# Kernel optimization log

Hardware: AMD Instinct MI355X
Metric: run time of the kernel (lower is better)

The kernel has to match this reference:

```python
import jax, jax.numpy as jnp
import numpy as np
from jax import lax

B, L, STEPS = 64, 512, 20


def setup_inputs() -> dict:
    key = jax.random.key(0)
    k1, k2, k3, k4 = jax.random.split(key, 4)
    scores = jax.random.uniform(k1, (B, L, L), dtype=jnp.float32)
    # M is a hard 0/1 constraint mask in the original pipeline; make it binary + symmetric
    m_raw = jax.random.uniform(k2, (B, L, L), dtype=jnp.float32)
    M = (m_raw > 0.5).astype(jnp.float32)
    M = jnp.maximum(M, jnp.swapaxes(M, 1, 2))
    return {
        "scores": scores,
        "M": M,
        "s": jnp.float32(0.5),
        "w": jax.random.uniform(k3, (1,), dtype=jnp.float32),
        "rho_p": jax.random.uniform(k4, (L, L), dtype=jnp.float32),
        "alpha": jnp.float32(0.005),
        "belt": jnp.float32(0.05),
        "lr_alpha": jnp.float32(0.99),
        "lr_belt": jnp.float32(0.99),
    }


def reference(scores, M, s, w, rho_p, alpha, belt, lr_alpha, lr_belt):
    relu = jax.nn.relu

    def sym(x):  # (x + x^T)/2 * M, transpose over the two seq dims
        return (x + jnp.swapaxes(x, 1, 2)) * 0.5 * M

    U = scores - s                      # [B,L,L]
    A_hat = scores
    A = sym(A_hat)
    Lm = w * relu(jnp.sum(A, axis=-1) - 1.0)  # [B,L]

    def step(carry, t):
        Lm, A, A_hat = carry
        row_dev = jnp.sum(A, axis=-1) - 1.0                      # [B,L]
        G = U * 0.5 - (Lm * jnp.sign(row_dev))[:, :, None]       # broadcast replaces repeat
        a_t = alpha * jnp.power(lr_alpha, t)
        A_hat2 = A_hat + a_t * A_hat * M * (G + jnp.swapaxes(G, 1, 2))
        A_hat2 = relu(jnp.abs(A_hat2) - rho_p * a_t)
        A_hat2 = 1.0 - relu(1.0 - A_hat2)                        # clip above at 1
        A2 = sym(A_hat2)
        Lm2 = Lm + belt * jnp.power(lr_belt, t) * relu(jnp.sum(A2, axis=-1) - 1.0)
        return (Lm2, A2, A_hat2), None

    ts = jnp.arange(STEPS, dtype=scores.dtype)
    (Lm, A, A_hat), _ = lax.scan(step, (Lm, A, A_hat), ts)
    return A
```

## Files before the change

kernel.cpp:

```cpp
#include <hip/hip_runtime.h>
#include <cstdint>
#include <cstddef>

#define LDIM 512
#define BATCH 64
#define NSTEPS 20
#define NTHREADS 256
#define PTHREADS 512
#define SLABS 8
#define BPB 8
#define CNT_STRIDE 16

using f4 = __attribute__((ext_vector_type(4))) float;
using h4 = __attribute__((ext_vector_type(4))) _Float16;

#define MU_MASKED (-1024.0f)
#define MU_THRESH (-512.0f)

__device__ __forceinline__ float relu_f(float x) { return fmaxf(x, 0.0f); }
__device__ __forceinline__ float sign_f(float x) {
  return (x > 0.0f) ? 1.0f : ((x < 0.0f) ? -1.0f : 0.0f);
}
__device__ __forceinline__ float wave_reduce_sum(float v) {
  v += __shfl_xor(v, 32);
  v += __shfl_xor(v, 16);
  v += __shfl_xor(v, 8);
  v += __shfl_xor(v, 4);
  v += __shfl_xor(v, 2);
  v += __shfl_xor(v, 1);
  return v;
}
__device__ __forceinline__ void st_agent(float* p, float v) {
  __hip_atomic_store(p, v, __ATOMIC_RELAXED, __HIP_MEMORY_SCOPE_AGENT);
}
__device__ __forceinline__ float ld_agent(const float* p) {
  return __hip_atomic_load(p, __ATOMIC_RELAXED, __HIP_MEMORY_SCOPE_AGENT);
}

__global__ __launch_bounds__(NTHREADS) void k_build(
    const float* __restrict__ scores, const float* __restrict__ M,
    const float* __restrict__ s_ptr, _Float16* __restrict__ MU,
    unsigned int* __restrict__ counter) {
  __shared__ float Sa[64][65];
  __shared__ float Sb[64][65];
  if (blockIdx.x < BATCH && threadIdx.x == 0) counter[blockIdx.x * CNT_STRIDE] = 0u;
  const int b = blockIdx.x / 36;
  int rem = blockIdx.x % 36;
  int ti = 0;
  while (rem >= 8 - ti) {
    rem -= 8 - ti;
    ti++;
  }
  const int tj = ti + rem;
  const int tid = threadIdx.x;
  const int c = tid & 63;
  const int r0 = tid >> 6;
  const float sval = s_ptr[0];
  const size_t mb = (size_t)b * LDIM * LDIM;
#pragma unroll
  for (int k = 0; k < 16; k++) {
    const int r = 4 * k + r0;
    Sa[r][c] = scores[mb + (size_t)(ti * 64 + r) * LDIM + tj * 64 + c];
    Sb[r][c] = scores[mb + (size_t)(tj * 64 + r) * LDIM + ti * 64 + c];
  }
  __syncthreads();
#pragma unroll
  for (int k = 0; k < 16; k++) {
    const int r = 4 * k + r0;
    const size_t idx_ij = mb + (size_t)(ti * 64 + r) * LDIM + tj * 64 + c;
    const float mij = M[idx_ij];
    const float us = 0.5f * (Sa[r][c] + Sb[c][r]) - sval;
    MU[idx_ij] = (_Float16)((mij != 0.0f) ? us : MU_MASKED);
    if (ti != tj) {
      const size_t idx_ji = mb + (size_t)(tj * 64 + r) * LDIM + ti * 64 + c;
      const float mji = M[idx_ji];
      const float usj = 0.5f * (Sb[r][c] + Sa[c][r]) - sval;
      MU[idx_ji] = (_Float16)((mji != 0.0f) ? usj : MU_MASKED);
    }
  }
}

__global__ __launch_bounds__(NTHREADS) void k_rho(const float* __restrict__ rho,
                                                  _Float16* __restrict__ rho_h) {
  const int idx = (blockIdx.x * NTHREADS + threadIdx.x) * 4;
  const f4 v = *(const f4*)(rho + idx);
  h4 o;
#pragma unroll
  for (int k = 0; k < 4; k++) o[k] = (_Float16)v[k];
  *(h4*)(rho_h + idx) = o;
}

__global__ __launch_bounds__(PTHREADS, 2) void k_persist(
    const float* __restrict__ scores, const _Float16* __restrict__ MU,
    const _Float16* __restrict__ rho_h, const float* __restrict__ w_ptr,
    const float* __restrict__ alpha_ptr, const float* __restrict__ belt_ptr,
    const float* __restrict__ lra_ptr, const float* __restrict__ lrb_ptr,
    float* __restrict__ rowpart, float* __restrict__ colpart,
    unsigned int* __restrict__ counter, float* __restrict__ Ah) {
  __shared__ _Float16 muL[64][LDIM];
  __shared__ float stage[4][LDIM];
  __shared__ float lmsgS[LDIM];

  const int tid = threadIdx.x;
  const int lane = tid & 63;
  const int w = tid >> 6;
  const int b = blockIdx.x >> 3;
  const int sb = blockIdx.x & 7;
  const int wrow = sb * 64 + w * 8;
  const int j0 = lane << 2;
  const size_t mb = (size_t)b * LDIM * LDIM;

  const float wv = w_ptr[0];
  const float belt = belt_ptr[0];
  const float lra = lra_ptr[0];
  const float lrb = lrb_ptr[0];
  float at = alpha_ptr[0];
  float lrbp = 1.0f;
  float lm_reg = 0.0f;

  const size_t RP = (size_t)BATCH * LDIM;
  const size_t CP = (size_t)BATCH * SLABS * LDIM;
  unsigned int* const cnt = counter + b * CNT_STRIDE;

  f4 ahv[8][2];
  float colacc[8];

#define ARRIVE_WAIT(tgt)                                                       \
  do {                                                                         \
    __syncthreads();                                                           \
    if (tid == 0) {                                                            \
      __hip_atomic_fetch_add(cnt, 1u, __ATOMIC_RELEASE,                        \
                             __HIP_MEMORY_SCOPE_AGENT);                        \
      while (__hip_atomic_load(cnt, __ATOMIC_RELAXED,                          \
                               __HIP_MEMORY_SCOPE_AGENT) < (tgt))              \
        __builtin_amdgcn_s_sleep(8);                                           \
    }                                                                          \
    __syncthreads();                                                           \
  } while (0)

#define COLREDUCE_STORE(dstp)                                                  \
  do {                                                                         \
    if (w < 4) {                                                               \
      f4 sa = {colacc[0], colacc[1], colacc[2], colacc[3]};                    \
      f4 sbv = {colacc[4], colacc[5], colacc[6], colacc[7]};                   \
      *(f4*)&stage[w][j0] = sa;                                                \
      *(f4*)&stage[w][256 + j0] = sbv;                                         \
    }                                                                          \
    __syncthreads();                                                           \
    if (w >= 4) {                                                              \
      f4 sa = *(f4*)&stage[w - 4][j0];                                         \
      f4 sbv = *(f4*)&stage[w - 4][256 + j0];                                  \
      sa[0] += colacc[0]; sa[1] += colacc[1];                                  \
      sa[2] += colacc[2]; sa[3] += colacc[3];                                  \
      sbv[0] += colacc[4]; sbv[1] += colacc[5];                                \
      sbv[2] += colacc[6]; sbv[3] += colacc[7];                                \
      *(f4*)&stage[w - 4][j0] = sa;                                            \
      *(f4*)&stage[w - 4][256 + j0] = sbv;                                     \
    }                                                                          \
    __syncthreads();                                                           \
    {                                                                          \
      float cs = stage[0][tid] + stage[1][tid] + stage[2][tid] +               \
                 stage[3][tid];                                                \
      st_agent((dstp) + tid, cs);                                              \
    }                                                                          \
  } while (0)

#pragma unroll
  for (int k = 0; k < 8; k++) colacc[k] = 0.0f;
#pragma unroll
  for (int r = 0; r < 8; r++) {
    const int i = wrow + r;
    const size_t base = mb + (size_t)i * LDIM;
    const f4 s0 = *(const f4*)(scores + base + j0);
    const f4 s1 = *(const f4*)(scores + base + 256 + j0);
    const h4 m0 = *(const h4*)(MU + base + j0);
    const h4 m1 = *(const h4*)(MU + base + 256 + j0);
    ahv[r][0] = s0;
    ahv[r][1] = s1;
    const int lr = (w << 3) + r;
    *(h4*)&muL[lr][j0] = m0;
    *(h4*)&muL[lr][256 + j0] = m1;
    float rowc = 0.0f;
#pragma unroll
    for (int k = 0; k < 4; k++) {
      const float c0v = ((float)m0[k] > MU_THRESH) ? s0[k] : 0.0f;
      const float c1v = ((float)m1[k] > MU_THRESH) ? s1[k] : 0.0f;
      rowc += c0v + c1v;
      colacc[k] += c0v;
      colacc[4 + k] += c1v;
    }
    const float rsum = wave_reduce_sum(rowc);
    if (lane == 0) st_agent(rowpart + (size_t)b * LDIM + i, rsum);
  }
  COLREDUCE_STORE(colpart + ((size_t)b * SLABS + sb) * LDIM);
  ARRIVE_WAIT((unsigned)BPB);

  for (int sp = 0; sp < NSTEPS; ++sp) {
    const int par = sp & 1;
    {
      const int i = tid;
      const float rsum = ld_agent(rowpart + (size_t)par * RP + (size_t)b * LDIM + i);
      const float* cb = colpart + (size_t)par * CP + (size_t)b * SLABS * LDIM + i;
      float csum = 0.0f;
#pragma unroll
      for (int s2 = 0; s2 < SLABS; s2++) csum += ld_agent(cb + (size_t)s2 * LDIM);
      const float rd = 0.5f * (rsum + csum) - 1.0f;
      float lm;
      if (sp == 0)
        lm = wv * relu_f(rd);
      else
        lm = lm_reg + belt * lrbp * relu_f(rd);
      lm_reg = lm;
      lmsgS[i] = lm * sign_f(rd);
    }
    __syncthreads();

    const f4 lmja = *(const f4*)&lmsgS[j0];
    const f4 lmjb = *(const f4*)&lmsgS[256 + j0];
    const bool last = (sp == NSTEPS - 1);
    const float rat = at;
#pragma unroll
    for (int k = 0; k < 8; k++) colacc[k] = 0.0f;

#pragma unroll
    for (int r = 0; r < 8; r++) {
      const int i = wrow + r;
      const int lr = (w << 3) + r;
      const float lmi = lmsgS[i];
      const h4 mh0 = *(const h4*)&muL[lr][j0];
      const h4 mh1 = *(const h4*)&muL[lr][256 + j0];
      const h4 rh0 = *(const h4*)(rho_h + (size_t)i * LDIM + j0);
      const h4 rh1 = *(const h4*)(rho_h + (size_t)i * LDIM + 256 + j0);
      float rowc = 0.0f;
#pragma unroll
      for (int k = 0; k < 4; k++) {
        const float mva = (float)mh0[k];
        const bool ma = mva > MU_THRESH;
        const float ga = ma ? (mva - lmi - lmja[k]) : 0.0f;
        const float ua = ahv[r][0][k] * fmaf(rat, ga, 1.0f);
        const float va = fminf(relu_f(fabsf(ua) - (float)rh0[k] * rat), 1.0f);
        ahv[r][0][k] = va;
        const float ca = ma ? va : 0.0f;
        rowc += ca;
        colacc[k] += ca;
        const float mvb = (float)mh1[k];
        const bool mbk = mvb > MU_THRESH;
        const float gb = mbk ? (mvb - lmi - lmjb[k]) : 0.0f;
        const float ub = ahv[r][1][k] * fmaf(rat, gb, 1.0f);
        const float vb = fminf(relu_f(fabsf(ub) - (float)rh1[k] * rat), 1.0f);
        ahv[r][1][k] = vb;
        const float cbv = mbk ? vb : 0.0f;
        rowc += cbv;
        colacc[4 + k] += cbv;
      }
      if (!last) {
        const float rsum = wave_reduce_sum(rowc);
        if (lane == 0)
          st_agent(rowpart + (size_t)(par ^ 1) * RP + (size_t)b * LDIM + i, rsum);
      }
    }
    if (!last) {
      COLREDUCE_STORE(colpart + (size_t)(par ^ 1) * CP +
                      ((size_t)b * SLABS + sb) * LDIM);
      ARRIVE_WAIT((unsigned)BPB * (unsigned)(sp + 2));
    }
    at *= lra;
    if (sp > 0) lrbp *= lrb;
  }

#pragma unroll
  for (int r = 0; r < 8; r++) {
    const size_t base = mb + (size_t)(wrow + r) * LDIM;
    *(f4*)(Ah + base + j0) = ahv[r][0];
    *(f4*)(Ah + base + 256 + j0) = ahv[r][1];
  }
#undef ARRIVE_WAIT
#undef COLREDUCE_STORE
}

__global__ __launch_bounds__(NTHREADS) void k_final(float* __restrict__ Ah,
                                                    const float* __restrict__ M) {
  __shared__ float At[64][65];
  __shared__ float Bt[64][65];
  const int b = blockIdx.x / 36;
  int rem = blockIdx.x % 36;
  int ti = 0;
  while (rem >= 8 - ti) {
    rem -= 8 - ti;
    ti++;
  }
  const int tj = ti + rem;
  const int tid = threadIdx.x;
  const int c = tid & 63;
  const int r0 = tid >> 6;
  const size_t mb = (size_t)b * LDIM * LDIM;

#pragma unroll
  for (int k = 0; k < 16; k++) {
    const int r = 4 * k + r0;
    At[r][c] = Ah[mb + (size_t)(ti * 64 + r) * LDIM + tj * 64 + c];
    Bt[r][c] = Ah[mb + (size_t)(tj * 64 + r) * LDIM + ti * 64 + c];
  }
  __syncthreads();
#pragma unroll
  for (int k = 0; k < 16; k++) {
    const int r = 4 * k + r0;
    const size_t idx_ij = mb + (size_t)(ti * 64 + r) * LDIM + tj * 64 + c;
    const float mij = M[idx_ij];
    Ah[idx_ij] = 0.5f * (At[r][c] + Bt[c][r]) * mij;
    if (ti != tj) {
      const size_t idx_ji = mb + (size_t)(tj * 64 + r) * LDIM + ti * 64 + c;
      const float mji = M[idx_ji];
      Ah[idx_ji] = 0.5f * (Bt[r][c] + At[c][r]) * mji;
    }
  }
}

extern "C" void kernel_launch(void* const* d_in, const int* in_sizes, int n_in,
                              void* d_out, int out_size, void* d_ws,
                              size_t ws_size, hipStream_t stream) {
  const float* scores = (const float*)d_in[0];
  const float* M = (const float*)d_in[1];
  const float* s_p = (const float*)d_in[2];
  const float* w_p = (const float*)d_in[3];
  const float* rho = (const float*)d_in[4];
  const float* alpha_p = (const float*)d_in[5];
  const float* belt_p = (const float*)d_in[6];
  const float* lra_p = (const float*)d_in[7];
  const float* lrb_p = (const float*)d_in[8];
  float* Ah = (float*)d_out;

  char* ws = (char*)d_ws;
  size_t off = 0;
  auto walloc = [&](size_t bytes) -> void* {
    void* p = (void*)(ws + off);
    off += (bytes + 255) & ~(size_t)255;
    return p;
  };
  const size_t NEL = (size_t)BATCH * LDIM * LDIM;
  _Float16* MU = (_Float16*)walloc(NEL * 2);
  _Float16* rho_h = (_Float16*)walloc((size_t)LDIM * LDIM * 2);
  float* rowpart = (float*)walloc((size_t)2 * BATCH * LDIM * 4);
  float* colpart = (float*)walloc((size_t)2 * BATCH * SLABS * LDIM * 4);
  unsigned int* cnt = (unsigned int*)walloc(BATCH * CNT_STRIDE * 4);
  (void)in_sizes;
  (void)n_in;
  (void)out_size;
  (void)ws_size;

  k_build<<<dim3(BATCH * 36), dim3(NTHREADS), 0, stream>>>(scores, M, s_p, MU,
                                                           cnt);
  k_rho<<<dim3(LDIM * LDIM / (NTHREADS * 4)), dim3(NTHREADS), 0, stream>>>(
      rho, rho_h);

  k_persist<<<dim3(BATCH * BPB), dim3(PTHREADS), 0, stream>>>(
      scores, MU, rho_h, w_p, alpha_p, belt_p, lra_p, lrb_p, rowpart, colpart,
      cnt, Ah);

  k_final<<<dim3(BATCH * 36), dim3(NTHREADS), 0, stream>>>(Ah, M);
}
```

Measured before the change: 542.3 us.

## Use 1024-thread persistent blocks, fuse rho conversion into build, vectorize build

The persistent kernel now runs 4 blocks of 1024 threads per batch, each holding 128 rows, instead of 8 blocks of 512. This halves the column-partial slabs and the number of blocks taking part in each per-batch barrier, but doubles the shared MU tile to 128 KB per block. The rho fp16 conversion is folded into k_build to drop one launch, and k_build's loads and stores now use 4-wide vectors with padded shared tiles. Sched barriers are added inside the row loops. The larger LDS footprint may cut occupancy, since launch_bounds still requests 2 blocks per CU.

```diff
diff --git a/kernel.cpp b/kernel.cpp
--- a/kernel.cpp
+++ b/kernel.cpp
@@ -6,9 +6,8 @@
 #define BATCH 64
 #define NSTEPS 20
 #define NTHREADS 256
-#define PTHREADS 512
-#define SLABS 8
-#define BPB 8
+#define PTHREADS 1024
+#define BPB 4
 #define CNT_STRIDE 16
 
 using f4 = __attribute__((ext_vector_type(4))) float;
@@ -40,10 +39,20 @@
 __global__ __launch_bounds__(NTHREADS) void k_build(
     const float* __restrict__ scores, const float* __restrict__ M,
     const float* __restrict__ s_ptr, _Float16* __restrict__ MU,
+    const float* __restrict__ rho, _Float16* __restrict__ rho_h,
     unsigned int* __restrict__ counter) {
-  __shared__ float Sa[64][65];
-  __shared__ float Sb[64][65];
-  if (blockIdx.x < BATCH && threadIdx.x == 0) counter[blockIdx.x * CNT_STRIDE] = 0u;
+  __shared__ float Sa[64][68];
+  __shared__ float Sb[64][68];
+  const int tid = threadIdx.x;
+  if (blockIdx.x < BATCH && tid == 0) counter[blockIdx.x * CNT_STRIDE] = 0u;
+  if (blockIdx.x < 256) {
+    const int idx = (blockIdx.x * NTHREADS + tid) * 4;
+    const f4 v = *(const f4*)(rho + idx);
+    h4 o;
+#pragma unroll
+    for (int k = 0; k < 4; k++) o[k] = (_Float16)v[k];
+    *(h4*)(rho_h + idx) = o;
+  }
   const int b = blockIdx.x / 36;
   int rem = blockIdx.x % 36;
   int ti = 0;
@@ -52,42 +61,44 @@
     ti++;
   }
   const int tj = ti + rem;
-  const int tid = threadIdx.x;
-  const int c = tid & 63;
-  const int r0 = tid >> 6;
+  const int cg = tid & 15;
+  const int rr = tid >> 4;
+  const int c4 = cg * 4;
   const float sval = s_ptr[0];
   const size_t mb = (size_t)b * LDIM * LDIM;
 #pragma unroll
-  for (int k = 0; k < 16; k++) {
-    const int r = 4 * k + r0;
-    Sa[r][c] = scores[mb + (size_t)(ti * 64 + r) * LDIM + tj * 64 + c];
-    Sb[r][c] = scores[mb + (size_t)(tj * 64 + r) * LDIM + ti * 64 + c];
+  for (int p = 0; p < 4; p++) {
+    const int r = p * 16 + rr;
+    *(f4*)&Sa[r][c4] =
+        *(const f4*)(scores + mb + (size_t)(ti * 64 + r) * LDIM + tj * 64 + c4);
+    *(f4*)&Sb[r][c4] =
+        *(const f4*)(scores + mb + (size_t)(tj * 64 + r) * LDIM + ti * 64 + c4);
   }
   __syncthreads();
 #pragma unroll
-  for (int k = 0; k < 16; k++) {
-    const int r = 4 * k + r0;
-    const size_t idx_ij = mb + (size_t)(ti * 64 + r) * LDIM + tj * 64 + c;
-    const float mij = M[idx_ij];
-    const float us = 0.5f * (Sa[r][c] + Sb[c][r]) - sval;
-    MU[idx_ij] = (_Float16)((mij != 0.0f) ? us : MU_MASKED);
+  for (int p = 0; p < 4; p++) {
+    const int r = p * 16 + rr;
+    const size_t idx_ij = mb + (size_t)(ti * 64 + r) * LDIM + tj * 64 + c4;
+    const f4 mij = *(const f4*)(M + idx_ij);
+    h4 o;
+#pragma unroll
+    for (int k = 0; k < 4; k++) {
+      const float us = 0.5f * (Sa[r][c4 + k] + Sb[c4 + k][r]) - sval;
+      o[k] = (_Float16)((mij[k] != 0.0f) ? us : MU_MASKED);
+    }
+    *(h4*)(MU + idx_ij) = o;
     if (ti != tj) {
-      const size_t idx_ji = mb + (size_t)(tj * 64 + r) * LDIM + ti * 64 + c;
-      const float mji = M[idx_ji];
-      const float usj = 0.5f * (Sb[r][c] + Sa[c][r]) - sval;
-      MU[idx_ji] = (_Float16)((mji != 0.0f) ? usj : MU_MASKED);
-    }
-  }
-}
-
-__global__ __launch_bounds__(NTHREADS) void k_rho(const float* __restrict__ rho,
-                                                  _Float16* __restrict__ rho_h) {
-  const int idx = (blockIdx.x * NTHREADS + threadIdx.x) * 4;
-  const f4 v = *(const f4*)(rho + idx);
-  h4 o;
-#pragma unroll
-  for (int k = 0; k < 4; k++) o[k] = (_Float16)v[k];
-  *(h4*)(rho_h + idx) = o;
+      const size_t idx_ji = mb + (size_t)(tj * 64 + r) * LDIM + ti * 64 + c4;
+      const f4 mji = *(const f4*)(M + idx_ji);
+      h4 oj;
+#pragma unroll
+      for (int k = 0; k < 4; k++) {
+        const float usj = 0.5f * (Sb[r][c4 + k] + Sa[c4 + k][r]) - sval;
+        oj[k] = (_Float16)((mji[k] != 0.0f) ? usj : MU_MASKED);
+      }
+      *(h4*)(MU + idx_ji) = oj;
+    }
+  }
 }
 
 __global__ __launch_bounds__(PTHREADS, 2) void k_persist(
@@ -97,16 +108,16 @@
     const float* __restrict__ lra_ptr, const float* __restrict__ lrb_ptr,
     float* __restrict__ rowpart, float* __restrict__ colpart,
     unsigned int* __restrict__ counter, float* __restrict__ Ah) {
-  __shared__ _Float16 muL[64][LDIM];
-  __shared__ float stage[4][LDIM];
+  __shared__ _Float16 muL[128][LDIM];
+  __shared__ float stage[8][LDIM];
   __shared__ float lmsgS[LDIM];
 
   const int tid = threadIdx.x;
   const int lane = tid & 63;
   const int w = tid >> 6;
-  const int b = blockIdx.x >> 3;
-  const int sb = blockIdx.x & 7;
-  const int wrow = sb * 64 + w * 8;
+  const int b = blockIdx.x >> 2;
+  const int sb = blockIdx.x & 3;
+  const int wrow = sb * 128 + w * 8;
   const int j0 = lane << 2;
   const size_t mb = (size_t)b * LDIM * LDIM;
 
@@ -119,7 +130,7 @@
   float lm_reg = 0.0f;
 
   const size_t RP = (size_t)BATCH * LDIM;
-  const size_t CP = (size_t)BATCH * SLABS * LDIM;
+  const size_t CP = (size_t)BATCH * BPB * LDIM;
   unsigned int* const cnt = counter + b * CNT_STRIDE;
 
   f4 ahv[8][2];
@@ -140,27 +151,28 @@
 
 #define COLREDUCE_STORE(dstp)                                                  \
   do {                                                                         \
-    if (w < 4) {                                                               \
+    if (w < 8) {                                                               \
       f4 sa = {colacc[0], colacc[1], colacc[2], colacc[3]};                    \
       f4 sbv = {colacc[4], colacc[5], colacc[6], colacc[7]};                   \
       *(f4*)&stage[w][j0] = sa;                                                \
       *(f4*)&stage[w][256 + j0] = sbv;                                         \
     }                                                                          \
     __syncthreads();                                                           \
-    if (w >= 4) {                                                              \
-      f4 sa = *(f4*)&stage[w - 4][j0];                                         \
-      f4 sbv = *(f4*)&stage[w - 4][256 + j0];                                  \
+    if (w >= 8) {                                                              \
+      f4 sa = *(f4*)&stage[w - 8][j0];                                         \
+      f4 sbv = *(f4*)&stage[w - 8][256 + j0];                                  \
       sa[0] += colacc[0]; sa[1] += colacc[1];                                  \
       sa[2] += colacc[2]; sa[3] += colacc[3];                                  \
       sbv[0] += colacc[4]; sbv[1] += colacc[5];                                \
       sbv[2] += colacc[6]; sbv[3] += colacc[7];                                \
-      *(f4*)&stage[w - 4][j0] = sa;                                            \
-      *(f4*)&stage[w - 4][256 + j0] = sbv;                                     \
+      *(f4*)&stage[w - 8][j0] = sa;                                            \
+      *(f4*)&stage[w - 8][256 + j0] = sbv;                                     \
     }                                                                          \
     __syncthreads();                                                           \
-    {                                                                          \
+    if (tid < LDIM) {                                                          \
       float cs = stage[0][tid] + stage[1][tid] + stage[2][tid] +               \
-                 stage[3][tid];                                                \
+                 stage[3][tid] + stage[4][tid] + stage[5][tid] +               \
+                 stage[6][tid] + stage[7][tid];                                \
       st_agent((dstp) + tid, cs);                                              \
     }                                                                          \
   } while (0)
@@ -191,19 +203,19 @@
     }
     const float rsum = wave_reduce_sum(rowc);
     if (lane == 0) st_agent(rowpart + (size_t)b * LDIM + i, rsum);
-  }
-  COLREDUCE_STORE(colpart + ((size_t)b * SLABS + sb) * LDIM);
+    if (r == 3) __builtin_amdgcn_sched_barrier(0);
+  }
+  COLREDUCE_STORE(colpart + ((size_t)b * BPB + sb) * LDIM);
   ARRIVE_WAIT((unsigned)BPB);
 
   for (int sp = 0; sp < NSTEPS; ++sp) {
     const int par = sp & 1;
-    {
+    if (tid < LDIM) {
       const int i = tid;
       const float rsum = ld_agent(rowpart + (size_t)par * RP + (size_t)b * LDIM + i);
-      const float* cb = colpart + (size_t)par * CP + (size_t)b * SLABS * LDIM + i;
-      float csum = 0.0f;
-#pragma unroll
-      for (int s2 = 0; s2 < SLABS; s2++) csum += ld_agent(cb + (size_t)s2 * LDIM);
+      const float* cb = colpart + (size_t)par * CP + (size_t)b * BPB * LDIM + i;
+      const float csum = ld_agent(cb) + ld_agent(cb + LDIM) +
+                         ld_agent(cb + 2 * LDIM) + ld_agent(cb + 3 * LDIM);
       const float rd = 0.5f * (rsum + csum) - 1.0f;
       float lm;
       if (sp == 0)
@@ -258,10 +270,11 @@
         if (lane == 0)
           st_agent(rowpart + (size_t)(par ^ 1) * RP + (size_t)b * LDIM + i, rsum);
       }
+      if (r == 3) __builtin_amdgcn_sched_barrier(0);
     }
     if (!last) {
       COLREDUCE_STORE(colpart + (size_t)(par ^ 1) * CP +
-                      ((size_t)b * SLABS + sb) * LDIM);
+                      ((size_t)b * BPB + sb) * LDIM);
       ARRIVE_WAIT((unsigned)BPB * (unsigned)(sp + 2));
     }
     at *= lra;
@@ -341,17 +354,15 @@
   _Float16* MU = (_Float16*)walloc(NEL * 2);
   _Float16* rho_h = (_Float16*)walloc((size_t)LDIM * LDIM * 2);
   float* rowpart = (float*)walloc((size_t)2 * BATCH * LDIM * 4);
-  float* colpart = (float*)walloc((size_t)2 * BATCH * SLABS * LDIM * 4);
+  float* colpart = (float*)walloc((size_t)2 * BATCH * BPB * LDIM * 4);
   unsigned int* cnt = (unsigned int*)walloc(BATCH * CNT_STRIDE * 4);
   (void)in_sizes;
   (void)n_in;
   (void)out_size;
   (void)ws_size;
 
-  k_build<<<dim3(BATCH * 36), dim3(NTHREADS), 0, stream>>>(scores, M, s_p, MU,
-                                                           cnt);
-  k_rho<<<dim3(LDIM * LDIM / (NTHREADS * 4)), dim3(NTHREADS), 0, stream>>>(
-      rho, rho_h);
+  k_build<<<dim3(BATCH * 36), dim3(NTHREADS), 0, stream>>>(
+      scores, M, s_p, MU, rho, rho_h, cnt);
 
   k_persist<<<dim3(BATCH * BPB), dim3(PTHREADS), 0, stream>>>(
       scores, MU, rho_h, w_p, alpha_p, belt_p, lra_p, lrb_p, rowpart, colpart,
```

Result: slower. 1.264 ms (+133.0%).
